# Performance work log

Measured on AMD Instinct MI355X. Metric: run time of the kernel, lower is better.

Reference implementation:

```python
import jax, jax.numpy as jnp
import numpy as np

ATTN_WINDOW = 7  # attention_window from attn_params; dilation (attention_stride) = 1


def _xavier(key, shape):
    lim = np.sqrt(6.0 / (shape[0] + shape[1]))
    return jax.random.uniform(key, shape, jnp.float32, -lim, lim)


def setup_inputs() -> dict:
    key = jax.random.key(0)
    ks = jax.random.split(key, 8)
    B, Cin, Him, Wim = 4, 3, 112, 112
    Cmid, Cout = 128, 128
    x = jax.random.normal(ks[0], (B, Cin, Him, Wim), jnp.float32)
    conv_w = jax.random.normal(ks[1], (Cmid, Cin, 3, 3), jnp.float32) * 0.1  # OIHW
    conv_b = jnp.zeros((Cmid,), jnp.float32)
    q_w = _xavier(ks[2], (Cmid, Cmid)); q_b = jnp.zeros((Cmid,), jnp.float32)
    k_w = _xavier(ks[3], (Cmid, Cmid)); k_b = jnp.zeros((Cmid,), jnp.float32)
    v_w = _xavier(ks[4], (Cout, Cmid)); v_b = jnp.zeros((Cout,), jnp.float32)
    return {"x": x, "conv_w": conv_w, "conv_b": conv_b,
            "q_w": q_w, "q_b": q_b, "k_w": k_w, "k_b": k_b, "v_w": v_w, "v_b": v_b}


def _neighbor_idx(n, ksz):
    # NATTEN-style neighborhood: centered window, clamped to stay inside the image.
    starts = jnp.clip(jnp.arange(n) - ksz // 2, 0, n - ksz)
    return starts[:, None] + jnp.arange(ksz)[None, :]  # [n, ksz]


def reference(x, conv_w, conv_b, q_w, q_b, k_w, k_b, v_w, v_b):
    # conv stem (3x3, stride 2, pad 1) + ReLU
    f = jax.lax.conv_general_dilated(
        x, conv_w, window_strides=(2, 2), padding=[(1, 1), (1, 1)],
        dimension_numbers=("NCHW", "OIHW", "NCHW"))
    f = jax.nn.relu(f + conv_b[None, :, None, None])
    f = f.transpose(0, 2, 3, 1)  # NHWC  [B,H,W,Cmid]
    # 1x1 convs == per-pixel linear layers
    q = f @ q_w.T + q_b
    k = f @ k_w.T + k_b
    v = f @ v_w.T + v_b
    B, H, W, C = q.shape
    ksz = min(ATTN_WINDOW, H, W)
    ksz -= 1 if ksz % 2 == 0 else 0
    ih = _neighbor_idx(H, ksz)  # [H, ksz]
    iw = _neighbor_idx(W, ksz)  # [W, ksz]
    # gather per-pixel neighborhoods: [B,H,W,ksz,ksz,C]
    kn = k[:, ih[:, None, :, None], iw[None, :, None, :], :]
    vn = v[:, ih[:, None, :, None], iw[None, :, None, :], :]
    scale = C ** -0.5
    logits = jnp.einsum("bhwc,bhwijc->bhwij", q * scale, kn)
    attn = jax.nn.softmax(logits.reshape(B, H, W, -1), axis=-1).reshape(logits.shape)
    out = jnp.einsum("bhwij,bhwijc->bhwc", attn, vn)  # [B,H,W,Cout]
    return out.transpose(0, 3, 1, 2)  # back to NCHW
```

## Files before the change

### kernel.cpp

```cpp
#include <hip/hip_runtime.h>
#include <hip/hip_bf16.h>
#include <math.h>

#define HW 56
#define PPI (HW*HW)
#define NB 4
#define C 128
#define NPIX (NB*PPI)

typedef __attribute__((ext_vector_type(8))) short short8;
typedef __attribute__((ext_vector_type(4))) float f32x4;

__device__ __forceinline__ short bfbits(float v) {
    __hip_bfloat16 hb = __float2bfloat16(v);
    return *reinterpret_cast<short*>(&hb);
}
__device__ __forceinline__ unsigned packbf(float a, float b) {
    return (unsigned)(unsigned short)bfbits(a) | ((unsigned)(unsigned short)bfbits(b) << 16);
}

__global__ __launch_bounds__(256) void prep_kernel(
    const float* __restrict__ cw,
    const float* __restrict__ qw, const float* __restrict__ kw,
    const float* __restrict__ vw,
    __hip_bfloat16* __restrict__ wcf, __hip_bfloat16* __restrict__ wqkv)
{
    int gid = blockIdx.x * 256 + threadIdx.x;
    if (blockIdx.x < 192) {
        int m   = gid >> 14;
        int r   = gid & 16383;
        int col = r >> 7;
        int k   = r & 127;
        const float* W = (m == 0) ? qw : (m == 1) ? kw : vw;
        int kk = k >> 5, hi = (k >> 3) & 3, j = k & 7;
        wqkv[m * 16384 + ((kk * 4 + hi) * 128 + col) * 8 + j] = __float2bfloat16(W[col * 128 + k]);
    } else {
        int idx = gid - 192 * 256;
        int hi = idx >> 10, cout = (idx >> 3) & 127, j = idx & 7;
        int k  = hi * 8 + j;
        float v = (k < 27) ? cw[cout * 27 + k] : 0.f;
        wcf[(hi * 128 + cout) * 8 + j] = __float2bfloat16(v);
    }
}

#define VPITCH 272
#define XPITCH 24
#define XCH    504

__global__ __launch_bounds__(256, 2) void fused_kernel(
    const float* __restrict__ x, const __hip_bfloat16* __restrict__ wcf,
    const float* __restrict__ cb, const __hip_bfloat16* __restrict__ wqkv,
    const float* __restrict__ qb, const float* __restrict__ kb,
    const float* __restrict__ vb, float* __restrict__ out)
{
    __shared__ __align__(16) short k_lds[112 * 128];
    __shared__ __align__(16) short vT[128 * 136];
    __shared__ __align__(16) short q_lds[16 * 128];
    __shared__ __align__(16) char  uni_s[16 * 116 * 4];
    __shared__ __align__(16) short attnW[16 * 136];
    short* f_ch    = (short*)uni_s;
    float* logit_s = (float*)uni_s;
    short* x_lds   = attnW;

    int t = threadIdx.x, lane = t & 63, wid = t >> 6;
    int r16 = lane & 15, hi = lane >> 4;

    int bx = blockIdx.x;
    int b  = bx / 196;
    int rr = bx % 196;
    int th = rr / 14, tw = rr % 14;
    int ih0 = min(max(th*4 - 3, 0), HW - 10);
    int iw0 = min(max(tw*4 - 3, 0), HW - 10);

    {
        int ihA = 2*ih0 - 1, iwA = 2*iw0 - 1;
        #pragma unroll
        for (int it = 0; it < 6; ++it) {
            int i = t + 256*it;
            if (i < 1512) {
                int ci = i / XCH, r = i % XCH;
                int row = r / XPITCH, col = r % XPITCH;
                int ih = ihA + row, iw = iwA + col;
                float xv = 0.f;
                if (col < 21 && ih >= 0 && ih < 112 && iw >= 0 && iw < 112)
                    xv = x[((size_t)(b*3 + ci)*112 + ih)*112 + iw];
                x_lds[i] = bfbits(xv);
            }
        }
    }

    for (int i = t; i < 1024; i += 256) {
        int c = i >> 3, j = i & 7;
        int hsw = (c >> 3) & 7;
        int unit = (14 + (j >> 2)) ^ hsw;
        *(unsigned*)((char*)vT + c*VPITCH + (unit << 4) + (j & 3)*4) = 0u;
    }

    int cout0 = (wid*2 + 0)*16 + r16;
    int cout1 = (wid*2 + 1)*16 + r16;
    short8 cbw0 = *(const short8*)((const short*)wcf + (hi*128 + cout0)*8);
    short8 cbw1 = *(const short8*)((const short*)wcf + (hi*128 + cout1)*8);
    float cbias0 = cb[cout0], cbias1 = cb[cout1];

    int  offb[8];
    bool vmask[8];
    #pragma unroll
    for (int j = 0; j < 8; ++j) {
        int k = hi*8 + j;
        int ci = k/9, r9 = k%9, kh = r9/3, kw_ = r9%3;
        offb[j]  = ci*XCH + kh*XPITCH + kw_;
        vmask[j] = (k < 27);
    }

    float kvbias[4];
    #pragma unroll
    for (int i = 0; i < 4; ++i) {
        int idx = wid*4 + i, mv = idx >> 3, ct = idx & 7, c = ct*16 + r16;
        kvbias[i] = mv ? vb[c] : kb[c];
    }
    float qbias[2];
    #pragma unroll
    for (int i = 0; i < 2; ++i) qbias[i] = qb[(wid*2 + i)*16 + r16];

    __syncthreads();

    auto conv_to_fch = [&](int hl, int wl) {
        int pb = hl*(2*XPITCH) + wl*2;
        short8 af;
        #pragma unroll
        for (int j = 0; j < 8; ++j)
            af[j] = vmask[j] ? x_lds[offb[j] + pb] : (short)0;
        #pragma unroll
        for (int ctl = 0; ctl < 2; ++ctl) {
            int cout   = ctl ? cout1  : cout0;
            short8 bw  = ctl ? cbw1   : cbw0;
            float bias = ctl ? cbias1 : cbias0;
            f32x4 acc = {0.f, 0.f, 0.f, 0.f};
            acc = __builtin_amdgcn_mfma_f32_16x16x32_bf16(af, bw, acc, 0, 0, 0);
            int colblk = cout >> 3, inb = (cout & 7)*2;
            #pragma unroll
            for (int rg = 0; rg < 4; ++rg) {
                int px = hi*4 + rg;
                *(short*)((char*)f_ch + px*256 + ((colblk ^ px) << 4) + inb)
                    = bfbits(fmaxf(acc[rg] + bias, 0.f));
            }
        }
    };

    for (int cc = 0; cc < 7; ++cc) {
        int nc = min(cc*16 + r16, 99);
        conv_to_fch(nc/10, nc%10);
        __syncthreads();

        short8 fa[4];
        #pragma unroll
        for (int kk = 0; kk < 4; ++kk)
            fa[kk] = *(const short8*)((char*)f_ch + r16*256 + (((kk*4 + hi) ^ r16) << 4));

        #pragma unroll
        for (int i = 0; i < 4; ++i) {
            int idx = wid*4 + i;
            int mv  = idx >> 3;
            int ct  = idx & 7;
            const short* wb = (const short*)wqkv + (1+mv)*16384 + hi*1024 + r16*8 + ct*128;
            f32x4 acc = {0.f, 0.f, 0.f, 0.f};
            acc = __builtin_amdgcn_mfma_f32_16x16x32_bf16(fa[0], *(const short8*)(wb),         acc, 0, 0, 0);
            acc = __builtin_amdgcn_mfma_f32_16x16x32_bf16(fa[1], *(const short8*)(wb +  4096), acc, 0, 0, 0);
            acc = __builtin_amdgcn_mfma_f32_16x16x32_bf16(fa[2], *(const short8*)(wb +  8192), acc, 0, 0, 0);
            acc = __builtin_amdgcn_mfma_f32_16x16x32_bf16(fa[3], *(const short8*)(wb + 12288), acc, 0, 0, 0);
            int c = ct*16 + r16;
            float bb = kvbias[i];
            if (mv == 0) {
                int swz = c >> 3;
                #pragma unroll
                for (int rg = 0; rg < 4; ++rg) {
                    int n = cc*16 + hi*4 + rg;
                    *(short*)((char*)k_lds + n*256 + ((swz ^ (n & 15)) << 4) + (c & 7)*2)
                        = bfbits(acc[rg] + bb);
                }
            } else {
                int n0 = cc*16 + hi*4;
                unsigned lo  = packbf(acc[0] + bb, acc[1] + bb);
                unsigned hi2 = packbf(acc[2] + bb, acc[3] + bb);
                int hsw = (c >> 3) & 7;
                int off = (2*n0) ^ (hsw << 4);
                *(uint2*)((char*)vT + c*VPITCH + off) = make_uint2(lo, hi2);
            }
        }
        __syncthreads();
    }

    {
        int ph = th*4 + (r16 >> 2), pw = tw*4 + (r16 & 3);
        conv_to_fch(ph - ih0, pw - iw0);
        __syncthreads();

        {
            unsigned* aw = (unsigned*)attnW;
            for (int i = t; i < 1088; i += 256) aw[i] = 0u;
        }

        short8 fa[4];
        #pragma unroll
        for (int kk = 0; kk < 4; ++kk)
            fa[kk] = *(const short8*)((char*)f_ch + r16*256 + (((kk*4 + hi) ^ r16) << 4));

        #pragma unroll
        for (int i = 0; i < 2; ++i) {
            int ct = wid*2 + i;
            const short* wb = (const short*)wqkv + hi*1024 + r16*8 + ct*128;
            f32x4 acc = {0.f, 0.f, 0.f, 0.f};
            acc = __builtin_amdgcn_mfma_f32_16x16x32_bf16(fa[0], *(const short8*)(wb),         acc, 0, 0, 0);
            acc = __builtin_amdgcn_mfma_f32_16x16x32_bf16(fa[1], *(const short8*)(wb +  4096), acc, 0, 0, 0);
            acc = __builtin_amdgcn_mfma_f32_16x16x32_bf16(fa[2], *(const short8*)(wb +  8192), acc, 0, 0, 0);
            acc = __builtin_amdgcn_mfma_f32_16x16x32_bf16(fa[3], *(const short8*)(wb + 12288), acc, 0, 0, 0);
            int c = ct*16 + r16;
            float bb = qbias[i];
            #pragma unroll
            for (int rg = 0; rg < 4; ++rg) {
                int px = hi*4 + rg;
                *(short*)((char*)q_lds + px*256 + (((c >> 3) ^ px) << 4) + (c & 7)*2)
                    = bfbits(acc[rg] + bb);
            }
        }
        __syncthreads();
    }

    short8 qa[4];
    #pragma unroll
    for (int kk = 0; kk < 4; ++kk)
        qa[kk] = *(const short8*)((char*)q_lds + r16*256 + (((kk*4 + hi) ^ r16) << 4));

    for (int nt = wid; nt < 7; nt += 4) {
        const char* kb_ = (const char*)k_lds + (nt*16 + r16)*256;
        f32x4 acc = {0.f, 0.f, 0.f, 0.f};
        #pragma unroll
        for (int kk = 0; kk < 4; ++kk) {
            short8 kv = *(const short8*)(kb_ + (((kk*4 + hi) ^ r16) << 4));
            acc = __builtin_amdgcn_mfma_f32_16x16x32_bf16(qa[kk], kv, acc, 0, 0, 0);
        }
        #pragma unroll
        for (int rg = 0; rg < 4; ++rg)
            logit_s[(hi*4 + rg)*116 + nt*16 + r16] = acc[rg];
    }
    __syncthreads();

    {
        int r7 = lane / 7, s7 = lane - 7*r7;
        bool valid = lane < 49;
        const float scale = 0.08838834764831845f;
        #pragma unroll
        for (int px = 0; px < 4; ++px) {
            int p = wid*4 + px;
            int h = th*4 + (p >> 2), w = tw*4 + (p & 3);
            int hs = min(max(h - 3, 0), HW - 7);
            int ws = min(max(w - 3, 0), HW - 7);
            int col = (hs - ih0 + r7)*10 + (ws - iw0 + s7);
            float lg = valid ? logit_s[p*116 + col] * scale : -INFINITY;
            float m = lg;
            #pragma unroll
            for (int d = 1; d < 64; d <<= 1) m = fmaxf(m, __shfl_xor(m, d));
            float e = valid ? __expf(lg - m) : 0.f;
            float s = e;
            #pragma unroll
            for (int d = 1; d < 64; d <<= 1) s += __shfl_xor(s, d);
            if (valid) {
                __hip_bfloat16 hb = __float2bfloat16(e / s);
                *(__hip_bfloat16*)((char*)attnW + p*VPITCH + 2*col) = hb;
            }
        }
    }
    __syncthreads();

    short8 pa[4];
    #pragma unroll
    for (int kk = 0; kk < 4; ++kk)
        pa[kk] = *(const short8*)((char*)attnW + r16*VPITCH + kk*64 + hi*16);

    for (int nt = wid; nt < 8; nt += 4) {
        int c   = nt*16 + r16;
        int hsw = (c >> 3) & 7;
        const char* vrow = (const char*)vT + c*VPITCH;
        f32x4 acc = {0.f, 0.f, 0.f, 0.f};
        #pragma unroll
        for (int kk = 0; kk < 4; ++kk) {
            short8 vbr = *(const short8*)(vrow + ((kk*64 + hi*16) ^ (hsw << 4)));
            acc = __builtin_amdgcn_mfma_f32_16x16x32_bf16(pa[kk], vbr, acc, 0, 0, 0);
        }
        #pragma unroll
        for (int rg = 0; rg < 4; ++rg) {
            int p = hi*4 + rg;
            int h = th*4 + (p >> 2), w = tw*4 + (p & 3);
            out[(((size_t)b*C + c)*HW + h)*HW + w] = acc[rg];
        }
    }
}

extern "C" void kernel_launch(void* const* d_in, const int* in_sizes, int n_in,
                              void* d_out, int out_size, void* d_ws, size_t ws_size,
                              hipStream_t stream) {
    const float* x      = (const float*)d_in[0];
    const float* conv_w = (const float*)d_in[1];
    const float* conv_b = (const float*)d_in[2];
    const float* q_w    = (const float*)d_in[3];
    const float* q_b    = (const float*)d_in[4];
    const float* k_w    = (const float*)d_in[5];
    const float* k_b    = (const float*)d_in[6];
    const float* v_w    = (const float*)d_in[7];
    const float* v_b    = (const float*)d_in[8];
    float* out = (float*)d_out;

    __hip_bfloat16* wqkv = (__hip_bfloat16*)d_ws;
    __hip_bfloat16* wcf  = wqkv + 3 * 16384;

    prep_kernel<<<208, 256, 0, stream>>>(conv_w, q_w, k_w, v_w, wcf, wqkv);
    fused_kernel<<<NB*196, 256, 0, stream>>>(x, wcf, conv_b, wqkv,
                                             q_b, k_b, v_b, out);
}
```

Measured before the change: 42.93 us.

## Fuse per-chunk QK logits into K projection loop and shrink LDS footprint

Q is now projected first and kept in registers. Each 16-key K chunk is projected into a small reused LDS buffer and immediately multiplied against Q, with the logits held in registers. The full 112-row K buffer and the logit scratch buffer go away, and softmax runs from registers using per-element window masks. The smaller LDS allocation is meant to let three blocks share a CU, signalled by the raised launch bound. In exchange, all four waves repeat the same QK MFMAs and softmax math, and register pressure rises.

```diff
diff --git a/kernel.cpp b/kernel.cpp
--- a/kernel.cpp
+++ b/kernel.cpp
@@ -47,20 +47,20 @@
 #define XPITCH 24
 #define XCH    504
 
-__global__ __launch_bounds__(256, 2) void fused_kernel(
+__global__ __launch_bounds__(256, 3) void fused_kernel(
     const float* __restrict__ x, const __hip_bfloat16* __restrict__ wcf,
     const float* __restrict__ cb, const __hip_bfloat16* __restrict__ wqkv,
     const float* __restrict__ qb, const float* __restrict__ kb,
     const float* __restrict__ vb, float* __restrict__ out)
 {
-    __shared__ __align__(16) short k_lds[112 * 128];
     __shared__ __align__(16) short vT[128 * 136];
-    __shared__ __align__(16) short q_lds[16 * 128];
-    __shared__ __align__(16) char  uni_s[16 * 116 * 4];
-    __shared__ __align__(16) short attnW[16 * 136];
-    short* f_ch    = (short*)uni_s;
-    float* logit_s = (float*)uni_s;
-    short* x_lds   = attnW;
+    __shared__ __align__(16) short poolA[16 * 128];
+    __shared__ __align__(16) short f_ch[16 * 128];
+    __shared__ __align__(16) short poolB[16 * 136];
+    short* q_lds   = poolA;
+    short* k_chunk = poolA;
+    short* x_lds   = poolB;
+    short* attnW   = poolB;
 
     int t = threadIdx.x, lane = t & 63, wid = t >> 6;
     int r16 = lane & 15, hi = lane >> 4;
@@ -147,6 +147,43 @@
         }
     };
 
+    short8 qa[4];
+    {
+        int ph = th*4 + (r16 >> 2), pw = tw*4 + (r16 & 3);
+        conv_to_fch(ph - ih0, pw - iw0);
+        __syncthreads();
+
+        short8 fa[4];
+        #pragma unroll
+        for (int kk = 0; kk < 4; ++kk)
+            fa[kk] = *(const short8*)((char*)f_ch + r16*256 + (((kk*4 + hi) ^ r16) << 4));
+
+        #pragma unroll
+        for (int i = 0; i < 2; ++i) {
+            int ct = wid*2 + i;
+            const short* wb = (const short*)wqkv + hi*1024 + r16*8 + ct*128;
+            f32x4 acc = {0.f, 0.f, 0.f, 0.f};
+            acc = __builtin_amdgcn_mfma_f32_16x16x32_bf16(fa[0], *(const short8*)(wb),         acc, 0, 0, 0);
+            acc = __builtin_amdgcn_mfma_f32_16x16x32_bf16(fa[1], *(const short8*)(wb +  4096), acc, 0, 0, 0);
+            acc = __builtin_amdgcn_mfma_f32_16x16x32_bf16(fa[2], *(const short8*)(wb +  8192), acc, 0, 0, 0);
+            acc = __builtin_amdgcn_mfma_f32_16x16x32_bf16(fa[3], *(const short8*)(wb + 12288), acc, 0, 0, 0);
+            int c = ct*16 + r16;
+            float bb = qbias[i];
+            #pragma unroll
+            for (int rg = 0; rg < 4; ++rg) {
+                int px = hi*4 + rg;
+                *(short*)((char*)q_lds + px*256 + (((c >> 3) ^ px) << 4) + (c & 7)*2)
+                    = bfbits(acc[rg] + bb);
+            }
+        }
+        __syncthreads();
+
+        #pragma unroll
+        for (int kk = 0; kk < 4; ++kk)
+            qa[kk] = *(const short8*)((char*)q_lds + r16*256 + (((kk*4 + hi) ^ r16) << 4));
+    }
+
+    float l[7][4];
     for (int cc = 0; cc < 7; ++cc) {
         int nc = min(cc*16 + r16, 99);
         conv_to_fch(nc/10, nc%10);
@@ -174,8 +211,8 @@
                 int swz = c >> 3;
                 #pragma unroll
                 for (int rg = 0; rg < 4; ++rg) {
-                    int n = cc*16 + hi*4 + rg;
-                    *(short*)((char*)k_lds + n*256 + ((swz ^ (n & 15)) << 4) + (c & 7)*2)
+                    int nl = hi*4 + rg;
+                    *(short*)((char*)k_chunk + nl*256 + ((swz ^ nl) << 4) + (c & 7)*2)
                         = bfbits(acc[rg] + bb);
                 }
             } else {
@@ -188,86 +225,58 @@
             }
         }
         __syncthreads();
+
+        {
+            const char* kbase = (const char*)k_chunk + r16*256;
+            f32x4 acc = {0.f, 0.f, 0.f, 0.f};
+            #pragma unroll
+            for (int kk = 0; kk < 4; ++kk) {
+                short8 kv = *(const short8*)(kbase + (((kk*4 + hi) ^ r16) << 4));
+                acc = __builtin_amdgcn_mfma_f32_16x16x32_bf16(qa[kk], kv, acc, 0, 0, 0);
+            }
+            #pragma unroll
+            for (int rg = 0; rg < 4; ++rg) l[cc][rg] = acc[rg];
+        }
     }
 
     {
-        int ph = th*4 + (r16 >> 2), pw = tw*4 + (r16 & 3);
-        conv_to_fch(ph - ih0, pw - iw0);
-        __syncthreads();
-
-        {
-            unsigned* aw = (unsigned*)attnW;
-            for (int i = t; i < 1088; i += 256) aw[i] = 0u;
-        }
-
-        short8 fa[4];
-        #pragma unroll
-        for (int kk = 0; kk < 4; ++kk)
-            fa[kk] = *(const short8*)((char*)f_ch + r16*256 + (((kk*4 + hi) ^ r16) << 4));
-
-        #pragma unroll
-        for (int i = 0; i < 2; ++i) {
-            int ct = wid*2 + i;
-            const short* wb = (const short*)wqkv + hi*1024 + r16*8 + ct*128;
-            f32x4 acc = {0.f, 0.f, 0.f, 0.f};
-            acc = __builtin_amdgcn_mfma_f32_16x16x32_bf16(fa[0], *(const short8*)(wb),         acc, 0, 0, 0);
-            acc = __builtin_amdgcn_mfma_f32_16x16x32_bf16(fa[1], *(const short8*)(wb +  4096), acc, 0, 0, 0);
-            acc = __builtin_amdgcn_mfma_f32_16x16x32_bf16(fa[2], *(const short8*)(wb +  8192), acc, 0, 0, 0);
-            acc = __builtin_amdgcn_mfma_f32_16x16x32_bf16(fa[3], *(const short8*)(wb + 12288), acc, 0, 0, 0);
-            int c = ct*16 + r16;
-            float bb = qbias[i];
-            #pragma unroll
-            for (int rg = 0; rg < 4; ++rg) {
-                int px = hi*4 + rg;
-                *(short*)((char*)q_lds + px*256 + (((c >> 3) ^ px) << 4) + (c & 7)*2)
-                    = bfbits(acc[rg] + bb);
-            }
-        }
-        __syncthreads();
-    }
-
-    short8 qa[4];
-    #pragma unroll
-    for (int kk = 0; kk < 4; ++kk)
-        qa[kk] = *(const short8*)((char*)q_lds + r16*256 + (((kk*4 + hi) ^ r16) << 4));
-
-    for (int nt = wid; nt < 7; nt += 4) {
-        const char* kb_ = (const char*)k_lds + (nt*16 + r16)*256;
-        f32x4 acc = {0.f, 0.f, 0.f, 0.f};
-        #pragma unroll
-        for (int kk = 0; kk < 4; ++kk) {
-            short8 kv = *(const short8*)(kb_ + (((kk*4 + hi) ^ r16) << 4));
-            acc = __builtin_amdgcn_mfma_f32_16x16x32_bf16(qa[kk], kv, acc, 0, 0, 0);
-        }
-        #pragma unroll
-        for (int rg = 0; rg < 4; ++rg)
-            logit_s[(hi*4 + rg)*116 + nt*16 + r16] = acc[rg];
-    }
-    __syncthreads();
-
-    {
-        int r7 = lane / 7, s7 = lane - 7*r7;
-        bool valid = lane < 49;
         const float scale = 0.08838834764831845f;
         #pragma unroll
-        for (int px = 0; px < 4; ++px) {
-            int p = wid*4 + px;
-            int h = th*4 + (p >> 2), w = tw*4 + (p & 3);
-            int hs = min(max(h - 3, 0), HW - 7);
-            int ws = min(max(w - 3, 0), HW - 7);
-            int col = (hs - ih0 + r7)*10 + (ws - iw0 + s7);
-            float lg = valid ? logit_s[p*116 + col] * scale : -INFINITY;
-            float m = lg;
-            #pragma unroll
-            for (int d = 1; d < 64; d <<= 1) m = fmaxf(m, __shfl_xor(m, d));
-            float e = valid ? __expf(lg - m) : 0.f;
-            float s = e;
-            #pragma unroll
-            for (int d = 1; d < 64; d <<= 1) s += __shfl_xor(s, d);
-            if (valid) {
-                __hip_bfloat16 hb = __float2bfloat16(e / s);
-                *(__hip_bfloat16*)((char*)attnW + p*VPITCH + 2*col) = hb;
-            }
+        for (int rg = 0; rg < 4; ++rg) {
+            int px = hi*4 + rg;
+            int h = th*4 + (px >> 2), w = tw*4 + (px & 3);
+            int r0 = min(max(h - 3, 0), HW - 7) - ih0;
+            int c0 = min(max(w - 3, 0), HW - 7) - iw0;
+            float lv[7]; bool vn[7];
+            float m = -INFINITY;
+            #pragma unroll
+            for (int cc = 0; cc < 7; ++cc) {
+                int n  = cc*16 + r16;
+                int nr = n / 10, ncl = n - nr*10;
+                vn[cc] = (n < 100) && ((unsigned)(nr - r0) < 7u) && ((unsigned)(ncl - c0) < 7u);
+                lv[cc] = l[cc][rg] * scale;
+                if (vn[cc]) m = fmaxf(m, lv[cc]);
+            }
+            #pragma unroll
+            for (int d = 1; d < 16; d <<= 1) m = fmaxf(m, __shfl_xor(m, d));
+            float e[7]; float s = 0.f;
+            #pragma unroll
+            for (int cc = 0; cc < 7; ++cc) {
+                e[cc] = vn[cc] ? __expf(lv[cc] - m) : 0.f;
+                s += e[cc];
+            }
+            #pragma unroll
+            for (int d = 1; d < 16; d <<= 1) s += __shfl_xor(s, d);
+            float rs = 1.f / s;
+            #pragma unroll
+            for (int cc = 0; cc < 7; ++cc) {
+                if ((cc & 3) == wid)
+                    *(short*)((char*)attnW + px*VPITCH + 2*(cc*16 + r16)) = bfbits(e[cc] * rs);
+            }
+        }
+        for (int i = t; i < 128; i += 256) {
+            int row = i >> 3, j = i & 7;
+            *(unsigned*)((char*)attnW + row*VPITCH + 224 + j*4) = 0u;
         }
     }
     __syncthreads();
```

Result: slower. 74.05 us (+72.5%).

## Compute Q first and stream K chunks into logits to shrink LDS

Applied to the files above, without the earlier changes.

Moves the query projection ahead of the K/V loop so each 16-row K chunk is multiplied against Q right after it is produced, instead of keeping all 112 K rows in shared memory. This drops the large k_lds buffer and reuses small pools for q, k chunks, x and attention weights, cutting LDS use enough to raise launch bounds from 2 to 3 blocks per CU. The cost is an extra Q/K MFMA step inside each chunk iteration, done by one wave at a time, and more register pressure from keeping qa live across the loop.

```diff
diff --git a/kernel.cpp b/kernel.cpp
--- a/kernel.cpp
+++ b/kernel.cpp
@@ -46,21 +46,23 @@
 #define VPITCH 272
 #define XPITCH 24
 #define XCH    504
-
-__global__ __launch_bounds__(256, 2) void fused_kernel(
+#define LPITCH 112
+
+__global__ __launch_bounds__(256, 3) void fused_kernel(
     const float* __restrict__ x, const __hip_bfloat16* __restrict__ wcf,
     const float* __restrict__ cb, const __hip_bfloat16* __restrict__ wqkv,
     const float* __restrict__ qb, const float* __restrict__ kb,
     const float* __restrict__ vb, float* __restrict__ out)
 {
-    __shared__ __align__(16) short k_lds[112 * 128];
     __shared__ __align__(16) short vT[128 * 136];
-    __shared__ __align__(16) short q_lds[16 * 128];
-    __shared__ __align__(16) char  uni_s[16 * 116 * 4];
-    __shared__ __align__(16) short attnW[16 * 136];
-    short* f_ch    = (short*)uni_s;
-    float* logit_s = (float*)uni_s;
-    short* x_lds   = attnW;
+    __shared__ __align__(16) short poolA[16 * 128];
+    __shared__ __align__(16) short f_ch[16 * 128];
+    __shared__ __align__(16) short poolB[16 * 136];
+    __shared__ __align__(16) float logit_s[16 * LPITCH];
+    short* q_lds   = poolA;
+    short* k_chunk = poolA;
+    short* x_lds   = poolB;
+    short* attnW   = poolB;
 
     int t = threadIdx.x, lane = t & 63, wid = t >> 6;
     int r16 = lane & 15, hi = lane >> 4;
@@ -146,6 +148,42 @@
             }
         }
     };
+
+    short8 qa[4];
+    {
+        int ph = th*4 + (r16 >> 2), pw = tw*4 + (r16 & 3);
+        conv_to_fch(ph - ih0, pw - iw0);
+        __syncthreads();
+
+        short8 fa[4];
+        #pragma unroll
+        for (int kk = 0; kk < 4; ++kk)
+            fa[kk] = *(const short8*)((char*)f_ch + r16*256 + (((kk*4 + hi) ^ r16) << 4));
+
+        #pragma unroll
+        for (int i = 0; i < 2; ++i) {
+            int ct = wid*2 + i;
+            const short* wb = (const short*)wqkv + hi*1024 + r16*8 + ct*128;
+            f32x4 acc = {0.f, 0.f, 0.f, 0.f};
+            acc = __builtin_amdgcn_mfma_f32_16x16x32_bf16(fa[0], *(const short8*)(wb),         acc, 0, 0, 0);
+            acc = __builtin_amdgcn_mfma_f32_16x16x32_bf16(fa[1], *(const short8*)(wb +  4096), acc, 0, 0, 0);
+            acc = __builtin_amdgcn_mfma_f32_16x16x32_bf16(fa[2], *(const short8*)(wb +  8192), acc, 0, 0, 0);
+            acc = __builtin_amdgcn_mfma_f32_16x16x32_bf16(fa[3], *(const short8*)(wb + 12288), acc, 0, 0, 0);
+            int c = ct*16 + r16;
+            float bb = qbias[i];
+            #pragma unroll
+            for (int rg = 0; rg < 4; ++rg) {
+                int px = hi*4 + rg;
+                *(short*)((char*)q_lds + px*256 + (((c >> 3) ^ px) << 4) + (c & 7)*2)
+                    = bfbits(acc[rg] + bb);
+            }
+        }
+        __syncthreads();
+
+        #pragma unroll
+        for (int kk = 0; kk < 4; ++kk)
+            qa[kk] = *(const short8*)((char*)q_lds + r16*256 + (((kk*4 + hi) ^ r16) << 4));
+    }
 
     for (int cc = 0; cc < 7; ++cc) {
         int nc = min(cc*16 + r16, 99);
@@ -174,8 +212,8 @@
                 int swz = c >> 3;
                 #pragma unroll
                 for (int rg = 0; rg < 4; ++rg) {
-                    int n = cc*16 + hi*4 + rg;
-                    *(short*)((char*)k_lds + n*256 + ((swz ^ (n & 15)) << 4) + (c & 7)*2)
+                    int nl = hi*4 + rg;
+                    *(short*)((char*)k_chunk + nl*256 + ((swz ^ nl) << 4) + (c & 7)*2)
                         = bfbits(acc[rg] + bb);
                 }
             } else {
@@ -188,60 +226,24 @@
             }
         }
         __syncthreads();
+
+        if ((cc & 3) == wid) {
+            const char* kbase = (const char*)k_chunk + r16*256;
+            f32x4 acc = {0.f, 0.f, 0.f, 0.f};
+            #pragma unroll
+            for (int kk = 0; kk < 4; ++kk) {
+                short8 kv = *(const short8*)(kbase + (((kk*4 + hi) ^ r16) << 4));
+                acc = __builtin_amdgcn_mfma_f32_16x16x32_bf16(qa[kk], kv, acc, 0, 0, 0);
+            }
+            #pragma unroll
+            for (int rg = 0; rg < 4; ++rg)
+                logit_s[(hi*4 + rg)*LPITCH + cc*16 + r16] = acc[rg];
+        }
     }
 
     {
-        int ph = th*4 + (r16 >> 2), pw = tw*4 + (r16 & 3);
-        conv_to_fch(ph - ih0, pw - iw0);
-        __syncthreads();
-
-        {
-            unsigned* aw = (unsigned*)attnW;
-            for (int i = t; i < 1088; i += 256) aw[i] = 0u;
-        }
-
-        short8 fa[4];
-        #pragma unroll
-        for (int kk = 0; kk < 4; ++kk)
-            fa[kk] = *(const short8*)((char*)f_ch + r16*256 + (((kk*4 + hi) ^ r16) << 4));
-
-        #pragma unroll
-        for (int i = 0; i < 2; ++i) {
-            int ct = wid*2 + i;
-            const short* wb = (const short*)wqkv + hi*1024 + r16*8 + ct*128;
-            f32x4 acc = {0.f, 0.f, 0.f, 0.f};
-            acc = __builtin_amdgcn_mfma_f32_16x16x32_bf16(fa[0], *(const short8*)(wb),         acc, 0, 0, 0);
-            acc = __builtin_amdgcn_mfma_f32_16x16x32_bf16(fa[1], *(const short8*)(wb +  4096), acc, 0, 0, 0);
-            acc = __builtin_amdgcn_mfma_f32_16x16x32_bf16(fa[2], *(const short8*)(wb +  8192), acc, 0, 0, 0);
-            acc = __builtin_amdgcn_mfma_f32_16x16x32_bf16(fa[3], *(const short8*)(wb + 12288), acc, 0, 0, 0);
-            int c = ct*16 + r16;
-            float bb = qbias[i];
-            #pragma unroll
-            for (int rg = 0; rg < 4; ++rg) {
-                int px = hi*4 + rg;
-                *(short*)((char*)q_lds + px*256 + (((c >> 3) ^ px) << 4) + (c & 7)*2)
-                    = bfbits(acc[rg] + bb);
-            }
-        }
-        __syncthreads();
-    }
-
-    short8 qa[4];
-    #pragma unroll
-    for (int kk = 0; kk < 4; ++kk)
-        qa[kk] = *(const short8*)((char*)q_lds + r16*256 + (((kk*4 + hi) ^ r16) << 4));
-
-    for (int nt = wid; nt < 7; nt += 4) {
-        const char* kb_ = (const char*)k_lds + (nt*16 + r16)*256;
-        f32x4 acc = {0.f, 0.f, 0.f, 0.f};
-        #pragma unroll
-        for (int kk = 0; kk < 4; ++kk) {
-            short8 kv = *(const short8*)(kb_ + (((kk*4 + hi) ^ r16) << 4));
-            acc = __builtin_amdgcn_mfma_f32_16x16x32_bf16(qa[kk], kv, acc, 0, 0, 0);
-        }
-        #pragma unroll
-        for (int rg = 0; rg < 4; ++rg)
-            logit_s[(hi*4 + rg)*116 + nt*16 + r16] = acc[rg];
+        unsigned* aw = (unsigned*)attnW;
+        for (int i = t; i < 1088; i += 256) aw[i] = 0u;
     }
     __syncthreads();
 
@@ -256,7 +258,7 @@
             int hs = min(max(h - 3, 0), HW - 7);
             int ws = min(max(w - 3, 0), HW - 7);
             int col = (hs - ih0 + r7)*10 + (ws - iw0 + s7);
-            float lg = valid ? logit_s[p*116 + col] * scale : -INFINITY;
+            float lg = valid ? logit_s[p*LPITCH + col] * scale : -INFINITY;
             float m = lg;
             #pragma unroll
             for (int d = 1; d < 64; d <<= 1) m = fmaxf(m, __shfl_xor(m, d));
```

New measurement: 47.57 us. 10.8% more time.
